# Kernel optimization log

Measured on AMD Instinct MI355X. Metric: run time of the kernel, lower is better.

## Reference

```python
import jax, jax.numpy as jnp
import numpy as np

K = 3
STRIDE = 1
PAD = 1


def conv2d(x, w, b, stride=1, padding=0):
    out = jax.lax.conv_general_dilated(
        x, w, (stride, stride), [(padding, padding), (padding, padding)],
        dimension_numbers=('NCHW', 'OIHW', 'NCHW'))
    return out + b[None, :, None, None]


def setup_inputs() -> dict:
    key = jax.random.key(0)
    ks = jax.random.split(key, 12)
    n, m, k = 64, 64, K
    sc = 0.05
    inp = {
        'x': jax.random.normal(ks[0], (8, n, 128, 128), jnp.float32),
        # attention1: Conv(n->k^2, k, s, p), Conv(k^2->k^2, 1), Conv(k^2->k^2, 1)
        'a1w1': jax.random.normal(ks[1], (k * k, n, k, k), jnp.float32) * sc,
        'a1b1': jax.random.normal(ks[2], (k * k,), jnp.float32) * sc,
        'a1w2': jax.random.normal(ks[3], (k * k, k * k, 1, 1), jnp.float32) * sc,
        'a1b2': jax.random.normal(ks[4], (k * k,), jnp.float32) * sc,
        'a1w3': jax.random.normal(ks[5], (k * k, k * k, 1, 1), jnp.float32) * sc,
        'a1b3': jax.random.normal(ks[6], (k * k,), jnp.float32) * sc,
        # attention3 (dynamic bias): Conv(n->m,1), Conv(m->m,1) after global avg pool
        'a3w1': jax.random.normal(ks[7], (m, n, 1, 1), jnp.float32) * sc,
        'a3b1': jax.random.normal(ks[8], (m,), jnp.float32) * sc,
        'a3w2': jax.random.normal(ks[9], (m, m, 1, 1), jnp.float32) * sc,
        'a3b2': jax.random.normal(ks[10], (m,), jnp.float32) * sc,
        # main conv weight (m, n, k, k)
        'weight': jax.random.normal(ks[11], (m, n, k, k), jnp.float32) * sc,
    }
    return inp


def reference(x, a1w1, a1b1, a1w2, a1b2, a1w3, a1b3, a3w1, a3b1, a3w2, a3b2, weight):
    k, s, p = K, STRIDE, PAD
    b, n, H, W = x.shape
    m = weight.shape[0]
    # per-pixel kernel attention: (b, k^2, nH, nW) in ki*k+kj order
    a = jax.nn.relu(conv2d(x, a1w1, a1b1, s, p))
    a = jax.nn.relu(conv2d(a, a1w2, a1b2))
    atw = jax.nn.sigmoid(conv2d(a, a1w3, a1b3))
    # im2col: (b, n*k^2, nH, nW), channel-major (c, ki, kj) like torch.unfold
    patches = jax.lax.conv_general_dilated_patches(
        x, (k, k), (s, s), [(p, p), (p, p)],
        dimension_numbers=('NCHW', 'OIHW', 'NCHW'))
    _, _, nH, nW = patches.shape
    patches = patches.reshape(b, n, k * k, nH, nW)
    # attention weights are repeated across input channels (the .repeat in torch)
    atx = patches * atw[:, None]                      # (b, n, k2, nH, nW)
    w = weight.reshape(m, n, k * k)
    y = jnp.einsum('bnpij,mnp->bmij', atx, w)          # (b, m, nH, nW)
    # dynamic bias from global average pool
    g = jnp.mean(x, axis=(2, 3), keepdims=True)        # (b, n, 1, 1)
    bias = conv2d(jax.nn.relu(conv2d(g, a3w1, a3b1)), a3w2, a3b2)  # (b, m, 1, 1)
    return y + bias
```

## Files before the change

kernel.cpp:

```cpp
#include <hip/hip_runtime.h>
#include <hip/hip_bf16.h>
#include <math.h>

#define HW 128
#define NPIX (HW * HW)
#define NB 8

#define TROWS 8
#define TCOLS 32
#define HR2 10
#define HC2 34
#define NPXT (HR2 * HC2)

typedef __attribute__((ext_vector_type(8))) short bf16x8;
typedef __attribute__((ext_vector_type(4))) float f32x4;

static __device__ __forceinline__ short f2bf(float v) {
  union { float f; unsigned u; } a; a.f = v;
  unsigned r = a.u + 0x7fffu + ((a.u >> 16) & 1u);
  return (short)(r >> 16);
}
static __device__ __forceinline__ float bfbits2f(unsigned u) {
  union { unsigned u; float f; } a; a.u = u; return a.f;
}

__global__ __launch_bounds__(256) void k_pack(const float* __restrict__ wgt,
                                              const float* __restrict__ a1w1,
                                              short* __restrict__ Apack,
                                              short* __restrict__ A1pack) {
  int idx = blockIdx.x * 256 + threadIdx.x;
  if (idx < 9 * 64 * 64) {
    int p = idx >> 12, m = (idx >> 6) & 63, n = idx & 63;
    Apack[idx] = f2bf(wgt[(m * 64 + n) * 9 + p]);
  }
  if (idx < 9 * 16 * 64) {
    int p = idx >> 10, q = (idx >> 6) & 15, n = idx & 63;
    A1pack[idx] = (q < 9) ? f2bf(a1w1[(q * 64 + n) * 9 + p]) : (short)0;
  }
}

__global__ __launch_bounds__(256) void k_gpool(const float* __restrict__ x,
                                               float* __restrict__ g) {
  int bn = blockIdx.x;
  const float4* p = (const float4*)(x + (size_t)bn * NPIX);
  float s = 0.f;
  #pragma unroll 4
  for (int i = threadIdx.x; i < NPIX / 4; i += 256) {
    float4 v = p[i];
    s += v.x + v.y + v.z + v.w;
  }
  #pragma unroll
  for (int o = 32; o > 0; o >>= 1) s += __shfl_down(s, o, 64);
  __shared__ float red[4];
  int lane = threadIdx.x & 63, wid = threadIdx.x >> 6;
  if (lane == 0) red[wid] = s;
  __syncthreads();
  if (threadIdx.x == 0)
    g[bn] = (red[0] + red[1] + red[2] + red[3]) * (1.0f / NPIX);
}

__global__ __launch_bounds__(64) void k_bias(const float* __restrict__ g,
                                             const float* __restrict__ a3w1,
                                             const float* __restrict__ a3b1,
                                             const float* __restrict__ a3w2,
                                             const float* __restrict__ a3b2,
                                             float* __restrict__ bias) {
  int b = blockIdx.x;
  int t = threadIdx.x;
  __shared__ float h[64];
  float s = a3b1[t];
  #pragma unroll
  for (int n = 0; n < 64; n++) s += a3w1[t * 64 + n] * g[b * 64 + n];
  h[t] = fmaxf(s, 0.f);
  __syncthreads();
  float s2 = a3b2[t];
  #pragma unroll
  for (int c = 0; c < 64; c++) s2 += a3w2[t * 64 + c] * h[c];
  bias[b * 64 + t] = s2;
}

__global__ __launch_bounds__(512, 4) void k_fused(
    const float* __restrict__ x, const short* __restrict__ Apack,
    const short* __restrict__ A1pack,
    const float* __restrict__ b1p, const float* __restrict__ w2p,
    const float* __restrict__ b2p, const float* __restrict__ w3p,
    const float* __restrict__ b3p,
    const float* __restrict__ bias, float* __restrict__ out) {
  __shared__ short xt[NPXT * 64];
  __shared__ float ab[TROWS][32][17];

  int b = blockIdx.y;
  int ty = blockIdx.x >> 2, tx = blockIdx.x & 3;
  int tid = threadIdx.x;
  int wid = tid >> 6, lane = tid & 63;
  int lp = lane & 15, kq = lane >> 4;
  int row0 = ty * TROWS, col0 = tx * TCOLS;
  const float* xb = x + (size_t)b * 64 * NPIX;

  for (int it = tid; it < NPXT * 64; it += 512) {
    int ch = it / NPXT;
    int pix = it - ch * NPXT;
    int r = pix / HC2;
    int c = pix - r * HC2;
    int gi = row0 - 1 + r, gj = col0 - 1 + c;
    float v = 0.f;
    if (gi >= 0 && gi < HW && gj >= 0 && gj < HW)
      v = xb[(size_t)ch * NPIX + gi * HW + gj];
    int byteoff = (pix * 128 + ch * 2) ^ ((pix & 7) << 4);
    *(short*)((char*)xt + byteoff) = f2bf(v);
  }
  __syncthreads();

  f32x4 acc1[2];
  #pragma unroll
  for (int g = 0; g < 2; g++) acc1[g] = (f32x4){0.f, 0.f, 0.f, 0.f};

  #pragma unroll
  for (int p = 0; p < 9; p++) {
    const int di = p / 3, dj = p % 3;
    int rt = wid + di;
    #pragma unroll
    for (int ck = 0; ck < 2; ck++) {
      bf16x8 af1 = *(const bf16x8*)(A1pack + (p * 16 + lp) * 64 + ck * 32 + kq * 8);
      #pragma unroll
      for (int g = 0; g < 2; g++) {
        int pix = rt * HC2 + g * 16 + lp + dj;
        int byteoff = (pix * 128 + ck * 64 + kq * 16) ^ ((pix & 7) << 4);
        bf16x8 bf = *(const bf16x8*)((const char*)xt + byteoff);
        acc1[g] = __builtin_amdgcn_mfma_f32_16x16x32_bf16(af1, bf, acc1[g], 0, 0, 0);
      }
    }
  }
  #pragma unroll
  for (int g = 0; g < 2; g++)
    #pragma unroll
    for (int r = 0; r < 4; r++)
      ab[wid][g * 16 + lp][kq * 4 + r] = acc1[g][r];
  __syncthreads();

  if (lane < 32) {
    float a[9], t1[9], t2[9];
    #pragma unroll
    for (int q = 0; q < 9; q++) a[q] = ab[wid][lane][q];
    #pragma unroll
    for (int q = 0; q < 9; q++) t1[q] = fmaxf(a[q] + b1p[q], 0.f);
    #pragma unroll
    for (int r = 0; r < 9; r++) {
      float s = b2p[r];
      #pragma unroll
      for (int q = 0; q < 9; q++) s += w2p[r * 9 + q] * t1[q];
      t2[r] = fmaxf(s, 0.f);
    }
    #pragma unroll
    for (int r = 0; r < 9; r++) {
      float s = b3p[r];
      #pragma unroll
      for (int q = 0; q < 9; q++) s += w3p[r * 9 + q] * t2[q];
      ab[wid][lane][r] = 1.f / (1.f + __expf(-s));
    }
  }
  __syncthreads();

  f32x4 acc[2][4];
  #pragma unroll
  for (int g = 0; g < 2; g++)
    #pragma unroll
    for (int mt = 0; mt < 4; mt++) acc[g][mt] = (f32x4){0.f, 0.f, 0.f, 0.f};

  #pragma unroll
  for (int p = 0; p < 9; p++) {
    const int di = p / 3, dj = p % 3;
    int rt = wid + di;
    bf16x8 frag[2][2];
    #pragma unroll
    for (int g = 0; g < 2; g++) {
      float awv = ab[wid][g * 16 + lp][p];
      int pix = rt * HC2 + g * 16 + lp + dj;
      #pragma unroll
      for (int ck = 0; ck < 2; ck++) {
        int byteoff = (pix * 128 + ck * 64 + kq * 16) ^ ((pix & 7) << 4);
        union { bf16x8 v; unsigned u[4]; } in, op;
        in.v = *(const bf16x8*)((const char*)xt + byteoff);
        #pragma unroll
        for (int d = 0; d < 4; d++) {
          float lo = bfbits2f(in.u[d] << 16) * awv;
          float hi = bfbits2f(in.u[d] & 0xffff0000u) * awv;
          __hip_bfloat162 pk = __float22bfloat162_rn(make_float2(lo, hi));
          union { __hip_bfloat162 h; unsigned u; } cv; cv.h = pk;
          op.u[d] = cv.u;
        }
        frag[g][ck] = op.v;
      }
    }
    #pragma unroll
    for (int mt = 0; mt < 4; mt++) {
      #pragma unroll
      for (int ck = 0; ck < 2; ck++) {
        bf16x8 af = *(const bf16x8*)(Apack + ((p * 64 + mt * 16 + lp) * 64 + ck * 32 + kq * 8));
        #pragma unroll
        for (int g = 0; g < 2; g++)
          acc[g][mt] = __builtin_amdgcn_mfma_f32_16x16x32_bf16(af, frag[g][ck], acc[g][mt], 0, 0, 0);
      }
    }
  }

  int i = row0 + wid;
  #pragma unroll
  for (int mt = 0; mt < 4; mt++) {
    #pragma unroll
    for (int r = 0; r < 4; r++) {
      int m = mt * 16 + kq * 4 + r;
      float bv = bias[b * 64 + m];
      #pragma unroll
      for (int g = 0; g < 2; g++) {
        int j = col0 + g * 16 + lp;
        out[(((size_t)b * 64 + m) * HW + i) * HW + j] = acc[g][mt][r] + bv;
      }
    }
  }
}

extern "C" void kernel_launch(void* const* d_in, const int* in_sizes, int n_in,
                              void* d_out, int out_size, void* d_ws, size_t ws_size,
                              hipStream_t stream) {
  const float* x    = (const float*)d_in[0];
  const float* a1w1 = (const float*)d_in[1];
  const float* a1b1 = (const float*)d_in[2];
  const float* a1w2 = (const float*)d_in[3];
  const float* a1b2 = (const float*)d_in[4];
  const float* a1w3 = (const float*)d_in[5];
  const float* a1b3 = (const float*)d_in[6];
  const float* a3w1 = (const float*)d_in[7];
  const float* a3b1 = (const float*)d_in[8];
  const float* a3w2 = (const float*)d_in[9];
  const float* a3b2 = (const float*)d_in[10];
  const float* wgt  = (const float*)d_in[11];
  float* out = (float*)d_out;

  float* ws = (float*)d_ws;
  float* g     = ws;
  float* bias  = g + NB * 64;
  short* Apack = (short*)(bias + NB * 64);
  short* A1pack = Apack + 9 * 64 * 64;

  k_pack<<<dim3(144), dim3(256), 0, stream>>>(wgt, a1w1, Apack, A1pack);
  k_gpool<<<dim3(NB * 64), dim3(256), 0, stream>>>(x, g);
  k_bias<<<dim3(NB), dim3(64), 0, stream>>>(g, a3w1, a3b1, a3w2, a3b2, bias);
  dim3 fgrid(64, NB);
  k_fused<<<fgrid, dim3(512), 0, stream>>>(x, Apack, A1pack,
                                           a1b1, a1w2, a1b2, a1w3, a1b3,
                                           bias, out);
}
```

Measured before the change: 84.25 us.

## Pre-transpose input to padded NHWC bf16 and fuse pooling into the transpose

```diff
diff --git a/kernel.cpp b/kernel.cpp
--- a/kernel.cpp
+++ b/kernel.cpp
@@ -5,12 +5,15 @@
 #define HW 128
 #define NPIX (HW * HW)
 #define NB 8
+#define PH 130
+#define PPIX (PH * PH)
 
 #define TROWS 8
 #define TCOLS 32
 #define HR2 10
 #define HC2 34
 #define NPXT (HR2 * HC2)
+#define ABST 20
 
 typedef __attribute__((ext_vector_type(8))) short bf16x8;
 typedef __attribute__((ext_vector_type(4))) float f32x4;
@@ -22,6 +25,11 @@
 }
 static __device__ __forceinline__ float bfbits2f(unsigned u) {
   union { unsigned u; float f; } a; a.u = u; return a.f;
+}
+static __device__ __forceinline__ unsigned pkbf2(float lo, float hi) {
+  __hip_bfloat162 pk = __float22bfloat162_rn(make_float2(lo, hi));
+  union { __hip_bfloat162 h; unsigned u; } cv; cv.h = pk;
+  return cv.u;
 }
 
 __global__ __launch_bounds__(256) void k_pack(const float* __restrict__ wgt,
@@ -36,6 +44,236 @@
   if (idx < 9 * 16 * 64) {
     int p = idx >> 10, q = (idx >> 6) & 15, n = idx & 63;
     A1pack[idx] = (q < 9) ? f2bf(a1w1[(q * 64 + n) * 9 + p]) : (short)0;
+  }
+}
+
+__global__ __launch_bounds__(256) void k_tr(const float* __restrict__ x,
+                                            short* __restrict__ xT,
+                                            float* __restrict__ part) {
+  int b = blockIdx.y;
+  int tid = threadIdx.x;
+  int wid = tid >> 6, lane = tid & 63;
+  int pix = (blockIdx.x << 8) + tid;
+  const float* xb = x + (size_t)b * 64 * NPIX + pix;
+  __shared__ float red[64][4];
+  unsigned pk[32];
+  #pragma unroll
+  for (int cp = 0; cp < 32; cp++) {
+    float v0 = xb[(size_t)(2 * cp) * NPIX];
+    float v1 = xb[(size_t)(2 * cp + 1) * NPIX];
+    pk[cp] = pkbf2(v0, v1);
+    float s0 = v0, s1 = v1;
+    #pragma unroll
+    for (int o = 32; o > 0; o >>= 1) {
+      s0 += __shfl_down(s0, o, 64);
+      s1 += __shfl_down(s1, o, 64);
+    }
+    if (lane == 0) { red[2 * cp][wid] = s0; red[2 * cp + 1][wid] = s1; }
+  }
+  int row = pix >> 7, col = pix & 127;
+  short* dst = xT + ((size_t)b * PPIX + (size_t)(row + 1) * PH + (col + 1)) * 64;
+  #pragma unroll
+  for (int q = 0; q < 8; q++)
+    *(uint4*)(dst + q * 8) =
+        make_uint4(pk[4 * q], pk[4 * q + 1], pk[4 * q + 2], pk[4 * q + 3]);
+  __syncthreads();
+  if (tid < 64)
+    part[((size_t)b * 64 + tid) * 64 + blockIdx.x] =
+        red[tid][0] + red[tid][1] + red[tid][2] + red[tid][3];
+}
+
+__global__ __launch_bounds__(256) void k_border(short* __restrict__ xT) {
+  int b = blockIdx.x;
+  for (int c = threadIdx.x; c < 4128; c += 256) {
+    int i = c >> 3, q = c & 7;
+    int gpix;
+    if (i < 130) gpix = i;
+    else if (i < 260) gpix = 129 * 130 + (i - 130);
+    else { int j = i - 260; gpix = (1 + (j >> 1)) * PH + ((j & 1) ? 129 : 0); }
+    *(uint4*)(xT + ((size_t)b * PPIX + gpix) * 64 + q * 8) = make_uint4(0, 0, 0, 0);
+  }
+}
+
+__global__ __launch_bounds__(256) void k_bias2(const float* __restrict__ part,
+                                               const float* __restrict__ a3w1,
+                                               const float* __restrict__ a3b1,
+                                               const float* __restrict__ a3w2,
+                                               const float* __restrict__ a3b2,
+                                               float* __restrict__ bias) {
+  int b = blockIdx.x;
+  int tid = threadIdx.x;
+  __shared__ float gsh[64], hsh[64];
+  int ch = tid >> 2, seg = tid & 3;
+  const float* pp = part + ((size_t)b * 64 + ch) * 64 + seg * 16;
+  float s = 0.f;
+  #pragma unroll
+  for (int k = 0; k < 16; k++) s += pp[k];
+  s += __shfl_down(s, 1, 4);
+  s += __shfl_down(s, 2, 4);
+  if (seg == 0) gsh[ch] = s * (1.0f / NPIX);
+  __syncthreads();
+  if (tid < 64) {
+    float t = a3b1[tid];
+    #pragma unroll
+    for (int n = 0; n < 64; n++) t += a3w1[tid * 64 + n] * gsh[n];
+    hsh[tid] = fmaxf(t, 0.f);
+  }
+  __syncthreads();
+  if (tid < 64) {
+    float s2 = a3b2[tid];
+    #pragma unroll
+    for (int c = 0; c < 64; c++) s2 += a3w2[tid * 64 + c] * hsh[c];
+    bias[b * 64 + tid] = s2;
+  }
+}
+
+__global__ __launch_bounds__(512, 4) void k_fused(
+    const short* __restrict__ xT, const short* __restrict__ Apack,
+    const short* __restrict__ A1pack,
+    const float* __restrict__ b1p, const float* __restrict__ w2p,
+    const float* __restrict__ b2p, const float* __restrict__ w3p,
+    const float* __restrict__ b3p,
+    const float* __restrict__ bias, float* __restrict__ out) {
+  __shared__ short xt[NPXT * 64];
+  __shared__ float ab[TROWS][32][ABST];
+
+  int b = blockIdx.y;
+  int ty = blockIdx.x >> 2, tx = blockIdx.x & 3;
+  int tid = threadIdx.x;
+  int wid = tid >> 6, lane = tid & 63;
+  int lp = lane & 15, kq = lane >> 4;
+  int row0 = ty * TROWS, col0 = tx * TCOLS;
+
+  {
+    const short* xTb = xT + (size_t)b * PPIX * 64;
+    int base = row0 * PH + col0;
+    for (int c = tid; c < NPXT * 8; c += 512) {
+      int pix = c >> 3;
+      int r = pix / HC2;
+      int col = pix - r * HC2;
+      bf16x8 v = *(const bf16x8*)(xTb + ((size_t)(base + r * PH + col)) * 64 + (c & 7) * 8);
+      int dst = (c * 16) ^ ((pix & 7) << 4);
+      *(bf16x8*)((char*)xt + dst) = v;
+    }
+  }
+  __syncthreads();
+
+  f32x4 acc1[2];
+  #pragma unroll
+  for (int g = 0; g < 2; g++) acc1[g] = (f32x4){0.f, 0.f, 0.f, 0.f};
+
+  #pragma unroll
+  for (int p = 0; p < 9; p++) {
+    const int di = p / 3, dj = p % 3;
+    int rt = wid + di;
+    #pragma unroll
+    for (int ck = 0; ck < 2; ck++) {
+      bf16x8 af1 = *(const bf16x8*)(A1pack + (p * 16 + lp) * 64 + ck * 32 + kq * 8);
+      #pragma unroll
+      for (int g = 0; g < 2; g++) {
+        int pix = rt * HC2 + g * 16 + lp + dj;
+        int byteoff = (pix * 128 + ck * 64 + kq * 16) ^ ((pix & 7) << 4);
+        bf16x8 bf = *(const bf16x8*)((const char*)xt + byteoff);
+        acc1[g] = __builtin_amdgcn_mfma_f32_16x16x32_bf16(af1, bf, acc1[g], 0, 0, 0);
+      }
+    }
+  }
+  #pragma unroll
+  for (int g = 0; g < 2; g++)
+    *(f32x4*)&ab[wid][g * 16 + lp][kq * 4] = acc1[g];
+  __syncthreads();
+
+  if (lane < 32) {
+    float a[9], t1[9], t2[9];
+    #pragma unroll
+    for (int q = 0; q < 9; q++) a[q] = ab[wid][lane][q];
+    #pragma unroll
+    for (int q = 0; q < 9; q++) t1[q] = fmaxf(a[q] + b1p[q], 0.f);
+    #pragma unroll
+    for (int r = 0; r < 9; r++) {
+      float s = b2p[r];
+      #pragma unroll
+      for (int q = 0; q < 9; q++) s += w2p[r * 9 + q] * t1[q];
+      t2[r] = fmaxf(s, 0.f);
+    }
+    #pragma unroll
+    for (int r = 0; r < 9; r++) {
+      float s = b3p[r];
+      #pragma unroll
+      for (int q = 0; q < 9; q++) s += w3p[r * 9 + q] * t2[q];
+      ab[wid][lane][r] = 1.f / (1.f + __expf(-s));
+    }
+  }
+  __syncthreads();
+
+  f32x4 acc[2][4];
+  #pragma unroll
+  for (int g = 0; g < 2; g++)
+    #pragma unroll
+    for (int mt = 0; mt < 4; mt++) acc[g][mt] = (f32x4){0.f, 0.f, 0.f, 0.f};
+
+  f32x4 awA[2], awB[2];
+  float awC[2];
+  #pragma unroll
+  for (int g = 0; g < 2; g++) {
+    const float* abp = &ab[wid][g * 16 + lp][0];
+    awA[g] = *(const f32x4*)abp;
+    awB[g] = *(const f32x4*)(abp + 4);
+    awC[g] = abp[8];
+  }
+
+  #pragma unroll
+  for (int p = 0; p < 9; p++) {
+    const int di = p / 3, dj = p % 3;
+    int rt = wid + di;
+    bf16x8 af[2][4];
+    #pragma unroll
+    for (int ck = 0; ck < 2; ck++)
+      #pragma unroll
+      for (int mt = 0; mt < 4; mt++)
+        af[ck][mt] = *(const bf16x8*)(Apack + ((p * 64 + mt * 16 + lp) * 64 + ck * 32 + kq * 8));
+
+    bf16x8 frag[2][2];
+    #pragma unroll
+    for (int g = 0; g < 2; g++) {
+      float awv = (p < 4) ? awA[g][p] : (p < 8) ? awB[g][p - 4] : awC[g];
+      int pix = rt * HC2 + g * 16 + lp + dj;
+      #pragma unroll
+      for (int ck = 0; ck < 2; ck++) {
+        int byteoff = (pix * 128 + ck * 64 + kq * 16) ^ ((pix & 7) << 4);
+        union { bf16x8 v; unsigned u[4]; } in, op;
+        in.v = *(const bf16x8*)((const char*)xt + byteoff);
+        #pragma unroll
+        for (int d = 0; d < 4; d++) {
+          float lo = bfbits2f(in.u[d] << 16) * awv;
+          float hi = bfbits2f(in.u[d] & 0xffff0000u) * awv;
+          op.u[d] = pkbf2(lo, hi);
+        }
+        frag[g][ck] = op.v;
+      }
+    }
+    #pragma unroll
+    for (int mt = 0; mt < 4; mt++)
+      #pragma unroll
+      for (int ck = 0; ck < 2; ck++)
+        #pragma unroll
+        for (int g = 0; g < 2; g++)
+          acc[g][mt] = __builtin_amdgcn_mfma_f32_16x16x32_bf16(af[ck][mt], frag[g][ck], acc[g][mt], 0, 0, 0);
+  }
+
+  int i = row0 + wid;
+  #pragma unroll
+  for (int mt = 0; mt < 4; mt++) {
+    #pragma unroll
+    for (int r = 0; r < 4; r++) {
+      int m = mt * 16 + kq * 4 + r;
+      float bv = bias[b * 64 + m];
+      #pragma unroll
+      for (int g = 0; g < 2; g++) {
+        int j = col0 + g * 16 + lp;
+        out[(((size_t)b * 64 + m) * HW + i) * HW + j] = acc[g][mt][r] + bv;
+      }
+    }
   }
 }
 
@@ -59,12 +297,12 @@
     g[bn] = (red[0] + red[1] + red[2] + red[3]) * (1.0f / NPIX);
 }
 
-__global__ __launch_bounds__(64) void k_bias(const float* __restrict__ g,
-                                             const float* __restrict__ a3w1,
-                                             const float* __restrict__ a3b1,
-                                             const float* __restrict__ a3w2,
-                                             const float* __restrict__ a3b2,
-                                             float* __restrict__ bias) {
+__global__ __launch_bounds__(64) void k_bias_old(const float* __restrict__ g,
+                                                 const float* __restrict__ a3w1,
+                                                 const float* __restrict__ a3b1,
+                                                 const float* __restrict__ a3w2,
+                                                 const float* __restrict__ a3b2,
+                                                 float* __restrict__ bias) {
   int b = blockIdx.x;
   int t = threadIdx.x;
   __shared__ float h[64];
@@ -79,7 +317,7 @@
   bias[b * 64 + t] = s2;
 }
 
-__global__ __launch_bounds__(512, 4) void k_fused(
+__global__ __launch_bounds__(512, 4) void k_fused_old(
     const float* __restrict__ x, const short* __restrict__ Apack,
     const short* __restrict__ A1pack,
     const float* __restrict__ b1p, const float* __restrict__ w2p,
@@ -114,7 +352,6 @@
   f32x4 acc1[2];
   #pragma unroll
   for (int g = 0; g < 2; g++) acc1[g] = (f32x4){0.f, 0.f, 0.f, 0.f};
-
   #pragma unroll
   for (int p = 0; p < 9; p++) {
     const int di = p / 3, dj = p % 3;
@@ -166,7 +403,6 @@
   for (int g = 0; g < 2; g++)
     #pragma unroll
     for (int mt = 0; mt < 4; mt++) acc[g][mt] = (f32x4){0.f, 0.f, 0.f, 0.f};
-
   #pragma unroll
   for (int p = 0; p < 9; p++) {
     const int di = p / 3, dj = p % 3;
@@ -185,15 +421,13 @@
         for (int d = 0; d < 4; d++) {
           float lo = bfbits2f(in.u[d] << 16) * awv;
           float hi = bfbits2f(in.u[d] & 0xffff0000u) * awv;
-          __hip_bfloat162 pk = __float22bfloat162_rn(make_float2(lo, hi));
-          union { __hip_bfloat162 h; unsigned u; } cv; cv.h = pk;
-          op.u[d] = cv.u;
+          op.u[d] = pkbf2(lo, hi);
         }
         frag[g][ck] = op.v;
       }
     }
     #pragma unroll
-    for (int mt = 0; mt < 4; mt++) {
+    for (int mt = 0; mt < 4; mt++)
       #pragma unroll
       for (int ck = 0; ck < 2; ck++) {
         bf16x8 af = *(const bf16x8*)(Apack + ((p * 64 + mt * 16 + lp) * 64 + ck * 32 + kq * 8));
@@ -201,7 +435,6 @@
         for (int g = 0; g < 2; g++)
           acc[g][mt] = __builtin_amdgcn_mfma_f32_16x16x32_bf16(af, frag[g][ck], acc[g][mt], 0, 0, 0);
       }
-    }
   }
 
   int i = row0 + wid;
@@ -237,17 +470,36 @@
   const float* wgt  = (const float*)d_in[11];
   float* out = (float*)d_out;
 
-  float* ws = (float*)d_ws;
-  float* g     = ws;
-  float* bias  = g + NB * 64;
-  short* Apack = (short*)(bias + NB * 64);
-  short* A1pack = Apack + 9 * 64 * 64;
-
-  k_pack<<<dim3(144), dim3(256), 0, stream>>>(wgt, a1w1, Apack, A1pack);
-  k_gpool<<<dim3(NB * 64), dim3(256), 0, stream>>>(x, g);
-  k_bias<<<dim3(NB), dim3(64), 0, stream>>>(g, a3w1, a3b1, a3w2, a3b2, bias);
-  dim3 fgrid(64, NB);
-  k_fused<<<fgrid, dim3(512), 0, stream>>>(x, Apack, A1pack,
-                                           a1b1, a1w2, a1b2, a1w3, a1b3,
-                                           bias, out);
-}
+  const size_t xT_sh   = (size_t)NB * PPIX * 64;
+  const size_t part_f  = (size_t)NB * 64 * 64;
+  const size_t need = xT_sh * 2 + part_f * 4 + 512 * 4 + (9 * 64 * 64 + 9 * 16 * 64) * 2;
+
+  if (ws_size >= need) {
+    short* xT    = (short*)d_ws;
+    float* part  = (float*)(xT + xT_sh);
+    float* bias  = part + part_f;
+    short* Apack = (short*)(bias + 512);
+    short* A1pack = Apack + 9 * 64 * 64;
+
+    k_pack<<<dim3(144), dim3(256), 0, stream>>>(wgt, a1w1, Apack, A1pack);
+    k_tr<<<dim3(64, NB), dim3(256), 0, stream>>>(x, xT, part);
+    k_border<<<dim3(NB), dim3(256), 0, stream>>>(xT);
+    k_bias2<<<dim3(NB), dim3(256), 0, stream>>>(part, a3w1, a3b1, a3w2, a3b2, bias);
+    k_fused<<<dim3(64, NB), dim3(512), 0, stream>>>(xT, Apack, A1pack,
+                                                    a1b1, a1w2, a1b2, a1w3, a1b3,
+                                                    bias, out);
+  } else {
+    float* ws = (float*)d_ws;
+    float* g     = ws;
+    float* bias  = g + NB * 64;
+    short* Apack = (short*)(bias + NB * 64);
+    short* A1pack = Apack + 9 * 64 * 64;
+
+    k_pack<<<dim3(144), dim3(256), 0, stream>>>(wgt, a1w1, Apack, A1pack);
+    k_gpool<<<dim3(NB * 64), dim3(256), 0, stream>>>(x, g);
+    k_bias_old<<<dim3(NB), dim3(64), 0, stream>>>(g, a3w1, a3b1, a3w2, a3b2, bias);
+    k_fused_old<<<dim3(64, NB), dim3(512), 0, stream>>>(x, Apack, A1pack,
+                                                        a1b1, a1w2, a1b2, a1w3, a1b3,
+                                                        bias, out);
+  }
+}
```

Result: slower. 89.37 us (+6.1%).

## Pre-transpose input to padded channels-last bf16 and restructure fused conv tiles

Applied to the files above, without the earlier changes.

```diff
diff --git a/kernel.cpp b/kernel.cpp
--- a/kernel.cpp
+++ b/kernel.cpp
@@ -5,12 +5,13 @@
 #define HW 128
 #define NPIX (HW * HW)
 #define NB 8
-
-#define TROWS 8
-#define TCOLS 32
-#define HR2 10
-#define HC2 34
-#define NPXT (HR2 * HC2)
+#define PH 130
+#define PPIX (PH * PH)
+
+#define HR3 4
+#define HC3 34
+#define NPXT3 (HR3 * HC3)
+#define NCHUNK (NPXT3 * 8)
 
 typedef __attribute__((ext_vector_type(8))) short bf16x8;
 typedef __attribute__((ext_vector_type(4))) float f32x4;
@@ -20,23 +21,65 @@
   unsigned r = a.u + 0x7fffu + ((a.u >> 16) & 1u);
   return (short)(r >> 16);
 }
-static __device__ __forceinline__ float bfbits2f(unsigned u) {
-  union { unsigned u; float f; } a; a.u = u; return a.f;
+static __device__ __forceinline__ unsigned pkbf2(float lo, float hi) {
+  __hip_bfloat162 pk = __float22bfloat162_rn(make_float2(lo, hi));
+  union { __hip_bfloat162 h; unsigned u; } cv; cv.h = pk;
+  return cv.u;
+}
+static __device__ __forceinline__ void gl_lds16(const void* g, void* l) {
+  __builtin_amdgcn_global_load_lds(
+      (const __attribute__((address_space(1))) unsigned int*)g,
+      (__attribute__((address_space(3))) unsigned int*)l, 16, 0, 0);
 }
 
 __global__ __launch_bounds__(256) void k_pack(const float* __restrict__ wgt,
                                               const float* __restrict__ a1w1,
                                               short* __restrict__ Apack,
-                                              short* __restrict__ A1pack) {
-  int idx = blockIdx.x * 256 + threadIdx.x;
-  if (idx < 9 * 64 * 64) {
-    int p = idx >> 12, m = (idx >> 6) & 63, n = idx & 63;
-    Apack[idx] = f2bf(wgt[(m * 64 + n) * 9 + p]);
-  }
-  if (idx < 9 * 16 * 64) {
-    int p = idx >> 10, q = (idx >> 6) & 15, n = idx & 63;
-    A1pack[idx] = (q < 9) ? f2bf(a1w1[(q * 64 + n) * 9 + p]) : (short)0;
-  }
+                                              short* __restrict__ A1pack,
+                                              short* __restrict__ xT) {
+  int bx = blockIdx.x;
+  if (bx < 144) {
+    int idx = bx * 256 + threadIdx.x;
+    if (idx < 9 * 64 * 64) {
+      int p = idx >> 12, m = (idx >> 6) & 63, n = idx & 63;
+      Apack[idx] = f2bf(wgt[(m * 64 + n) * 9 + p]);
+    }
+    if (idx < 9 * 16 * 64) {
+      int p = idx >> 10, q = (idx >> 6) & 15, n = idx & 63;
+      A1pack[idx] = (q < 9) ? f2bf(a1w1[(q * 64 + n) * 9 + p]) : (short)0;
+    }
+  } else {
+    int b = bx - 144;
+    for (int c = threadIdx.x; c < 4128; c += 256) {
+      int i = c >> 3, q = c & 7;
+      int gpix;
+      if (i < 130) gpix = i;
+      else if (i < 260) gpix = 129 * 130 + (i - 130);
+      else { int j = i - 260; gpix = (1 + (j >> 1)) * PH + ((j & 1) ? 129 : 0); }
+      *(uint4*)(xT + ((size_t)b * PPIX + gpix) * 64 + q * 8) = make_uint4(0, 0, 0, 0);
+    }
+  }
+}
+
+__global__ __launch_bounds__(256) void k_tr(const float* __restrict__ x,
+                                            short* __restrict__ xT) {
+  int b = blockIdx.y;
+  int tid = threadIdx.x;
+  int pix = (blockIdx.x << 8) + tid;
+  const float* xb = x + (size_t)b * 64 * NPIX + pix;
+  unsigned pk[32];
+  #pragma unroll
+  for (int cp = 0; cp < 32; cp++) {
+    float v0 = xb[(size_t)(2 * cp) * NPIX];
+    float v1 = xb[(size_t)(2 * cp + 1) * NPIX];
+    pk[cp] = pkbf2(v0, v1);
+  }
+  int row = pix >> 7, col = pix & 127;
+  short* dst = xT + ((size_t)b * PPIX + (size_t)(row + 1) * PH + (col + 1)) * 64;
+  #pragma unroll
+  for (int q = 0; q < 8; q++)
+    *(uint4*)(dst + q * 8) =
+        make_uint4(pk[4 * q], pk[4 * q + 1], pk[4 * q + 2], pk[4 * q + 3]);
 }
 
 __global__ __launch_bounds__(256) void k_gpool(const float* __restrict__ x,
@@ -79,69 +122,73 @@
   bias[b * 64 + t] = s2;
 }
 
-__global__ __launch_bounds__(512, 4) void k_fused(
-    const float* __restrict__ x, const short* __restrict__ Apack,
+__global__ __launch_bounds__(256, 6) void k_fused(
+    const short* __restrict__ xT, const short* __restrict__ Apack,
     const short* __restrict__ A1pack,
     const float* __restrict__ b1p, const float* __restrict__ w2p,
     const float* __restrict__ b2p, const float* __restrict__ w3p,
     const float* __restrict__ b3p,
     const float* __restrict__ bias, float* __restrict__ out) {
-  __shared__ short xt[NPXT * 64];
-  __shared__ float ab[TROWS][32][17];
-
-  int b = blockIdx.y;
-  int ty = blockIdx.x >> 2, tx = blockIdx.x & 3;
+  __shared__ short xt[NPXT3 * 64];
+
+  int bx = blockIdx.x;
+  int swz = (bx & 7) * 256 + (bx >> 3);
+  int b = swz >> 8;
+  int rem = swz & 255;
+  int ty = rem >> 2, tx = rem & 3;
+  int row0 = ty * 2, col0 = tx * 32;
+
   int tid = threadIdx.x;
   int wid = tid >> 6, lane = tid & 63;
   int lp = lane & 15, kq = lane >> 4;
-  int row0 = ty * TROWS, col0 = tx * TCOLS;
-  const float* xb = x + (size_t)b * 64 * NPIX;
-
-  for (int it = tid; it < NPXT * 64; it += 512) {
-    int ch = it / NPXT;
-    int pix = it - ch * NPXT;
-    int r = pix / HC2;
-    int c = pix - r * HC2;
-    int gi = row0 - 1 + r, gj = col0 - 1 + c;
-    float v = 0.f;
-    if (gi >= 0 && gi < HW && gj >= 0 && gj < HW)
-      v = xb[(size_t)ch * NPIX + gi * HW + gj];
-    int byteoff = (pix * 128 + ch * 2) ^ ((pix & 7) << 4);
-    *(short*)((char*)xt + byteoff) = f2bf(v);
+  int wr = wid >> 1, cg = wid & 1;
+
+  {
+    const short* xTb = xT + (size_t)b * PPIX * 64;
+    int base = row0 * PH + col0;
+    #pragma unroll
+    for (int it = 0; it < 4; it++) {
+      int c = it * 256 + tid;
+      int pix = c >> 3, q = c & 7;
+      int r = pix / HC3, col = pix - r * HC3;
+      int qs = q ^ (pix & 7);
+      const short* src = xTb + ((size_t)(base + r * PH + col)) * 64 + qs * 8;
+      void* ldst = (char*)xt + (it * 256 + wid * 64) * 16;
+      gl_lds16(src, ldst);
+    }
+    if (tid < 64) {
+      int c = 1024 + tid;
+      int pix = c >> 3, q = c & 7;
+      int r = pix / HC3, col = pix - r * HC3;
+      int qs = q ^ (pix & 7);
+      const short* src = xTb + ((size_t)(base + r * PH + col)) * 64 + qs * 8;
+      void* ldst = (char*)xt + 1024 * 16;
+      gl_lds16(src, ldst);
+    }
   }
   __syncthreads();
 
-  f32x4 acc1[2];
-  #pragma unroll
-  for (int g = 0; g < 2; g++) acc1[g] = (f32x4){0.f, 0.f, 0.f, 0.f};
-
+  f32x4 acc1 = (f32x4){0.f, 0.f, 0.f, 0.f};
   #pragma unroll
   for (int p = 0; p < 9; p++) {
     const int di = p / 3, dj = p % 3;
-    int rt = wid + di;
+    int pixb = (wr + di) * HC3 + cg * 16 + dj;
     #pragma unroll
     for (int ck = 0; ck < 2; ck++) {
       bf16x8 af1 = *(const bf16x8*)(A1pack + (p * 16 + lp) * 64 + ck * 32 + kq * 8);
-      #pragma unroll
-      for (int g = 0; g < 2; g++) {
-        int pix = rt * HC2 + g * 16 + lp + dj;
-        int byteoff = (pix * 128 + ck * 64 + kq * 16) ^ ((pix & 7) << 4);
-        bf16x8 bf = *(const bf16x8*)((const char*)xt + byteoff);
-        acc1[g] = __builtin_amdgcn_mfma_f32_16x16x32_bf16(af1, bf, acc1[g], 0, 0, 0);
-      }
-    }
-  }
-  #pragma unroll
-  for (int g = 0; g < 2; g++)
-    #pragma unroll
-    for (int r = 0; r < 4; r++)
-      ab[wid][g * 16 + lp][kq * 4 + r] = acc1[g][r];
-  __syncthreads();
-
-  if (lane < 32) {
+      int pix = pixb + lp;
+      int byteoff = (pix * 128 + ck * 64 + kq * 16) ^ ((pix & 7) << 4);
+      bf16x8 bf = *(const bf16x8*)((const char*)xt + byteoff);
+      acc1 = __builtin_amdgcn_mfma_f32_16x16x32_bf16(af1, bf, acc1, 0, 0, 0);
+    }
+  }
+
+  float aw[9];
+  {
     float a[9], t1[9], t2[9];
     #pragma unroll
-    for (int q = 0; q < 9; q++) a[q] = ab[wid][lane][q];
+    for (int q2 = 0; q2 < 9; q2++)
+      a[q2] = __shfl(acc1[q2 & 3], (q2 >> 2) * 16 + lp, 64);
     #pragma unroll
     for (int q = 0; q < 9; q++) t1[q] = fmaxf(a[q] + b1p[q], 0.f);
     #pragma unroll
@@ -156,66 +203,47 @@
       float s = b3p[r];
       #pragma unroll
       for (int q = 0; q < 9; q++) s += w3p[r * 9 + q] * t2[q];
-      ab[wid][lane][r] = 1.f / (1.f + __expf(-s));
-    }
-  }
-  __syncthreads();
-
-  f32x4 acc[2][4];
-  #pragma unroll
-  for (int g = 0; g < 2; g++)
-    #pragma unroll
-    for (int mt = 0; mt < 4; mt++) acc[g][mt] = (f32x4){0.f, 0.f, 0.f, 0.f};
+      aw[r] = 1.f / (1.f + __expf(-s));
+    }
+  }
+
+  f32x4 acc[4];
+  #pragma unroll
+  for (int mt = 0; mt < 4; mt++) acc[mt] = (f32x4){0.f, 0.f, 0.f, 0.f};
 
   #pragma unroll
   for (int p = 0; p < 9; p++) {
     const int di = p / 3, dj = p % 3;
-    int rt = wid + di;
-    bf16x8 frag[2][2];
-    #pragma unroll
-    for (int g = 0; g < 2; g++) {
-      float awv = ab[wid][g * 16 + lp][p];
-      int pix = rt * HC2 + g * 16 + lp + dj;
+    int pix = (wr + di) * HC3 + cg * 16 + dj + lp;
+    bf16x8 frag[2];
+    #pragma unroll
+    for (int ck = 0; ck < 2; ck++) {
+      int byteoff = (pix * 128 + ck * 64 + kq * 16) ^ ((pix & 7) << 4);
+      frag[ck] = *(const bf16x8*)((const char*)xt + byteoff);
+    }
+    float awp = aw[p];
+    #pragma unroll
+    for (int mt = 0; mt < 4; mt++) {
+      const short* ap = Apack + (p * 64 + mt * 16 + lp) * 64 + kq * 8;
+      bf16x8 af0 = *(const bf16x8*)(ap);
+      bf16x8 af1 = *(const bf16x8*)(ap + 32);
+      f32x4 tmp = (f32x4){0.f, 0.f, 0.f, 0.f};
+      tmp = __builtin_amdgcn_mfma_f32_16x16x32_bf16(af0, frag[0], tmp, 0, 0, 0);
+      tmp = __builtin_amdgcn_mfma_f32_16x16x32_bf16(af1, frag[1], tmp, 0, 0, 0);
       #pragma unroll
-      for (int ck = 0; ck < 2; ck++) {
-        int byteoff = (pix * 128 + ck * 64 + kq * 16) ^ ((pix & 7) << 4);
-        union { bf16x8 v; unsigned u[4]; } in, op;
-        in.v = *(const bf16x8*)((const char*)xt + byteoff);
-        #pragma unroll
-        for (int d = 0; d < 4; d++) {
-          float lo = bfbits2f(in.u[d] << 16) * awv;
-          float hi = bfbits2f(in.u[d] & 0xffff0000u) * awv;
-          __hip_bfloat162 pk = __float22bfloat162_rn(make_float2(lo, hi));
-          union { __hip_bfloat162 h; unsigned u; } cv; cv.h = pk;
-          op.u[d] = cv.u;
-        }
-        frag[g][ck] = op.v;
-      }
-    }
-    #pragma unroll
-    for (int mt = 0; mt < 4; mt++) {
-      #pragma unroll
-      for (int ck = 0; ck < 2; ck++) {
-        bf16x8 af = *(const bf16x8*)(Apack + ((p * 64 + mt * 16 + lp) * 64 + ck * 32 + kq * 8));
-        #pragma unroll
-        for (int g = 0; g < 2; g++)
-          acc[g][mt] = __builtin_amdgcn_mfma_f32_16x16x32_bf16(af, frag[g][ck], acc[g][mt], 0, 0, 0);
-      }
-    }
-  }
-
-  int i = row0 + wid;
+      for (int r = 0; r < 4; r++) acc[mt][r] += awp * tmp[r];
+    }
+  }
+
+  int i = row0 + wr;
+  int j = col0 + cg * 16 + lp;
   #pragma unroll
   for (int mt = 0; mt < 4; mt++) {
+    f32x4 bv = *(const f32x4*)(bias + b * 64 + mt * 16 + kq * 4);
     #pragma unroll
     for (int r = 0; r < 4; r++) {
       int m = mt * 16 + kq * 4 + r;
-      float bv = bias[b * 64 + m];
-      #pragma unroll
-      for (int g = 0; g < 2; g++) {
-        int j = col0 + g * 16 + lp;
-        out[(((size_t)b * 64 + m) * HW + i) * HW + j] = acc[g][mt][r] + bv;
-      }
+      out[(((size_t)b * 64 + m) * HW + i) * HW + j] = acc[mt][r] + bv[r];
     }
   }
 }
@@ -237,17 +265,18 @@
   const float* wgt  = (const float*)d_in[11];
   float* out = (float*)d_out;
 
-  float* ws = (float*)d_ws;
-  float* g     = ws;
-  float* bias  = g + NB * 64;
-  short* Apack = (short*)(bias + NB * 64);
+  const size_t xT_sh = (size_t)NB * PPIX * 64;
+  short* xT     = (short*)d_ws;
+  float* g      = (float*)(xT + xT_sh);
+  float* bias   = g + NB * 64;
+  short* Apack  = (short*)(bias + NB * 64);
   short* A1pack = Apack + 9 * 64 * 64;
 
-  k_pack<<<dim3(144), dim3(256), 0, stream>>>(wgt, a1w1, Apack, A1pack);
+  k_pack<<<dim3(152), dim3(256), 0, stream>>>(wgt, a1w1, Apack, A1pack, xT);
+  k_tr<<<dim3(64, NB), dim3(256), 0, stream>>>(x, xT);
   k_gpool<<<dim3(NB * 64), dim3(256), 0, stream>>>(x, g);
   k_bias<<<dim3(NB), dim3(64), 0, stream>>>(g, a3w1, a3b1, a3w2, a3b2, bias);
-  dim3 fgrid(64, NB);
-  k_fused<<<fgrid, dim3(512), 0, stream>>>(x, Apack, A1pack,
-                                           a1b1, a1w2, a1b2, a1w3, a1b3,
-                                           bias, out);
-}
+  k_fused<<<dim3(2048), dim3(256), 0, stream>>>(xT, Apack, A1pack,
+                                                a1b1, a1w2, a1b2, a1w3, a1b3,
+                                                bias, out);
+}
```

Result: slower. 141.4 us (+67.8%).
